# Kernel optimization log

Measured on AMD Instinct MI355X. Metric: run time of the kernel, lower is better.

The kernel has to match this reference:

```python
import jax, jax.numpy as jnp
import numpy as np

N, D = 131072, 512

def setup_inputs() -> dict:
    key = jax.random.key(0)
    kx, = jax.random.split(key, 1)
    X = jax.random.normal(kx, (N, D), dtype=jnp.float32)
    gamma = jnp.ones((D,), dtype=jnp.float32)
    beta = jnp.zeros((D,), dtype=jnp.float32)
    return {"X": X, "gamma": gamma, "beta": beta}

def reference(X, gamma, beta):
    # R = X - mean over rows (samples)
    R = X - jnp.mean(X, axis=0, keepdims=True)            # [N, D]
    # Sigma = diag(R^T @ R) / N  ==  per-feature biased variance
    Sigma = jnp.mean(R * R, axis=0)                       # [D]
    inv_sqrt_Sigma = jax.lax.rsqrt(Sigma)                 # [D] (no epsilon in original)
    Z = R * inv_sqrt_Sigma[None, :]                       # [N, D]
    Y = Z * gamma[None, :] + beta[None, :]                # [N, D]
    return Y
```

## Files before the change

### kernel.cpp

```cpp
#include <hip/hip_runtime.h>
#include <math.h>

#define N_ROWS 131072
#define D_COLS 512
#define TOTAL4 (N_ROWS * D_COLS / 4)

typedef float v4f __attribute__((ext_vector_type(4)));

__global__ __launch_bounds__(512)
void bn_stats_kernel(const v4f* __restrict__ X, float* __restrict__ partial) {
    const int t = threadIdx.x;
    const int g = blockIdx.x * blockDim.x + t;
    const int stride = gridDim.x * blockDim.x;

    v4f s = (v4f)0.0f;
    v4f q = (v4f)0.0f;

    for (int i = g; i < TOTAL4; i += stride) {
        v4f x = X[i];
        s += x;
        q += x * x;
    }

    __shared__ v4f ls[512];
    __shared__ v4f lq[512];
    ls[t] = s;
    lq[t] = q;
    __syncthreads();

    if (t < 256) {
        ls[t] += ls[t + 256];
        lq[t] += lq[t + 256];
    }
    __syncthreads();
    if (t < 128) {
        v4f sv = ls[t] + ls[t + 128];
        v4f qv = lq[t] + lq[t + 128];
        float* dst = partial + (size_t)blockIdx.x * 1024;
        *(v4f*)(dst + 4 * t)       = sv;
        *(v4f*)(dst + 512 + 4 * t) = qv;
    }
}

__global__ __launch_bounds__(256)
void bn_finalize_kernel(const float* __restrict__ partial,
                        const float* __restrict__ gamma,
                        const float* __restrict__ beta,
                        float* __restrict__ scale,
                        float* __restrict__ bias,
                        int B) {
    const int d = blockIdx.x;
    const int t = threadIdx.x;

    float s = 0.f, q = 0.f;
    for (int b = t; b < B; b += blockDim.x) {
        s += partial[(size_t)b * 1024 + d];
        q += partial[(size_t)b * 1024 + 512 + d];
    }

    __shared__ float ls[256];
    __shared__ float lq[256];
    ls[t] = s;
    lq[t] = q;
    __syncthreads();
    for (int off = 128; off > 0; off >>= 1) {
        if (t < off) { ls[t] += ls[t + off]; lq[t] += lq[t + off]; }
        __syncthreads();
    }

    if (t == 0) {
        const float invN = 1.0f / (float)N_ROWS;
        float mean = ls[0] * invN;
        float var  = lq[0] * invN - mean * mean;
        float inv  = rsqrtf(var);
        float sc   = gamma[d] * inv;
        scale[d] = sc;
        bias[d]  = beta[d] - mean * sc;
    }
}

__global__ __launch_bounds__(256)
void bn_norm_kernel(const v4f* __restrict__ X,
                    v4f* __restrict__ Y,
                    const float* __restrict__ scale,
                    const float* __restrict__ bias) {
    const int g = blockIdx.x * blockDim.x + threadIdx.x;
    const int stride = gridDim.x * blockDim.x;
    const int c = (g & 127) * 4;

    const v4f sc = *(const v4f*)(scale + c);
    const v4f bi = *(const v4f*)(bias + c);

    for (int i = g; i < TOTAL4; i += stride) {
        v4f x = X[i];
        v4f y = x * sc + bi;
        __builtin_nontemporal_store(y, &Y[i]);
    }
}

extern "C" void kernel_launch(void* const* d_in, const int* in_sizes, int n_in,
                              void* d_out, int out_size, void* d_ws, size_t ws_size,
                              hipStream_t stream) {
    const float* X     = (const float*)d_in[0];
    const float* gamma = (const float*)d_in[1];
    const float* beta  = (const float*)d_in[2];
    float* Y  = (float*)d_out;
    float* ws = (float*)d_ws;

    int B = 512;
    while (B > 64 && ((size_t)B * 1024 + 1024) * sizeof(float) > ws_size) B >>= 1;

    float* partial = ws;
    float* scale   = ws + (size_t)B * 1024;
    float* bias    = scale + 512;

    bn_stats_kernel<<<B, 512, 0, stream>>>((const v4f*)X, partial);
    bn_finalize_kernel<<<512, 256, 0, stream>>>(partial, gamma, beta, scale, bias, B);
    bn_norm_kernel<<<4096, 256, 0, stream>>>((const v4f*)X, (v4f*)Y, scale, bias);
}
```

Before: 479.0 us.

## Widen stats grid, unroll compile-time loops, vectorize finalize over feature quads

The stats kernel now runs 2048 blocks of 256 threads instead of 512 blocks of 512, with a compile-time trip count and unroll 8 to keep more loads in flight. The finalize kernel handles four features per block using vector loads and writes scale and bias into one packed buffer. The normalize kernel also gets a constant trip count with unroll 4. The wider stats grid means four times as many partial rows for finalize to read, and it needs a larger workspace, falling back to 512 blocks if the workspace is too small.

```diff
diff --git a/kernel.cpp b/kernel.cpp
--- a/kernel.cpp
+++ b/kernel.cpp
@@ -7,32 +7,30 @@
 
 typedef float v4f __attribute__((ext_vector_type(4)));
 
-__global__ __launch_bounds__(512)
+template<int NBLK>
+__global__ __launch_bounds__(256)
 void bn_stats_kernel(const v4f* __restrict__ X, float* __restrict__ partial) {
+    constexpr int STRIDE = NBLK * 256;
+    constexpr int ITERS  = TOTAL4 / STRIDE;
     const int t = threadIdx.x;
-    const int g = blockIdx.x * blockDim.x + t;
-    const int stride = gridDim.x * blockDim.x;
+    const int g = blockIdx.x * 256 + t;
 
     v4f s = (v4f)0.0f;
     v4f q = (v4f)0.0f;
 
-    for (int i = g; i < TOTAL4; i += stride) {
-        v4f x = X[i];
+    #pragma unroll 8
+    for (int k = 0; k < ITERS; ++k) {
+        v4f x = X[g + k * STRIDE];
         s += x;
         q += x * x;
     }
 
-    __shared__ v4f ls[512];
-    __shared__ v4f lq[512];
+    __shared__ v4f ls[256];
+    __shared__ v4f lq[256];
     ls[t] = s;
     lq[t] = q;
     __syncthreads();
 
-    if (t < 256) {
-        ls[t] += ls[t + 256];
-        lq[t] += lq[t + 256];
-    }
-    __syncthreads();
     if (t < 128) {
         v4f sv = ls[t] + ls[t + 128];
         v4f qv = lq[t] + lq[t + 128];
@@ -46,20 +44,20 @@
 void bn_finalize_kernel(const float* __restrict__ partial,
                         const float* __restrict__ gamma,
                         const float* __restrict__ beta,
-                        float* __restrict__ scale,
-                        float* __restrict__ bias,
+                        float* __restrict__ sb,
                         int B) {
-    const int d = blockIdx.x;
-    const int t = threadIdx.x;
+    const int qd = blockIdx.x;
+    const int t  = threadIdx.x;
 
-    float s = 0.f, q = 0.f;
-    for (int b = t; b < B; b += blockDim.x) {
-        s += partial[(size_t)b * 1024 + d];
-        q += partial[(size_t)b * 1024 + 512 + d];
+    v4f s = (v4f)0.0f, q = (v4f)0.0f;
+    for (int b = t; b < B; b += 256) {
+        const float* src = partial + (size_t)b * 1024;
+        s += *(const v4f*)(src + 4 * qd);
+        q += *(const v4f*)(src + 512 + 4 * qd);
     }
 
-    __shared__ float ls[256];
-    __shared__ float lq[256];
+    __shared__ v4f ls[256];
+    __shared__ v4f lq[256];
     ls[t] = s;
     lq[t] = q;
     __syncthreads();
@@ -70,31 +68,41 @@
 
     if (t == 0) {
         const float invN = 1.0f / (float)N_ROWS;
-        float mean = ls[0] * invN;
-        float var  = lq[0] * invN - mean * mean;
-        float inv  = rsqrtf(var);
-        float sc   = gamma[d] * inv;
-        scale[d] = sc;
-        bias[d]  = beta[d] - mean * sc;
+        v4f sv = ls[0], qv = lq[0];
+        v4f mean = sv * invN;
+        v4f var  = qv * invN - mean * mean;
+        v4f inv;
+        inv.x = rsqrtf(var.x);
+        inv.y = rsqrtf(var.y);
+        inv.z = rsqrtf(var.z);
+        inv.w = rsqrtf(var.w);
+        v4f g4 = *(const v4f*)(gamma + 4 * qd);
+        v4f b4 = *(const v4f*)(beta  + 4 * qd);
+        v4f sc = g4 * inv;
+        v4f bi = b4 - mean * sc;
+        *(v4f*)(sb + 4 * qd)       = sc;
+        *(v4f*)(sb + 512 + 4 * qd) = bi;
     }
 }
 
+template<int NBLK>
 __global__ __launch_bounds__(256)
 void bn_norm_kernel(const v4f* __restrict__ X,
                     v4f* __restrict__ Y,
-                    const float* __restrict__ scale,
-                    const float* __restrict__ bias) {
-    const int g = blockIdx.x * blockDim.x + threadIdx.x;
-    const int stride = gridDim.x * blockDim.x;
+                    const float* __restrict__ sb) {
+    constexpr int STRIDE = NBLK * 256;
+    constexpr int ITERS  = TOTAL4 / STRIDE;
+    const int g = blockIdx.x * 256 + threadIdx.x;
     const int c = (g & 127) * 4;
 
-    const v4f sc = *(const v4f*)(scale + c);
-    const v4f bi = *(const v4f*)(bias + c);
+    const v4f sc = *(const v4f*)(sb + c);
+    const v4f bi = *(const v4f*)(sb + 512 + c);
 
-    for (int i = g; i < TOTAL4; i += stride) {
-        v4f x = X[i];
+    #pragma unroll 4
+    for (int k = 0; k < ITERS; ++k) {
+        v4f x = X[g + k * STRIDE];
         v4f y = x * sc + bi;
-        __builtin_nontemporal_store(y, &Y[i]);
+        __builtin_nontemporal_store(y, &Y[g + k * STRIDE]);
     }
 }
 
@@ -107,14 +115,17 @@
     float* Y  = (float*)d_out;
     float* ws = (float*)d_ws;
 
-    int B = 512;
-    while (B > 64 && ((size_t)B * 1024 + 1024) * sizeof(float) > ws_size) B >>= 1;
+    int B = 2048;
+    if (((size_t)B * 1024 + 1024) * sizeof(float) > ws_size) B = 512;
 
     float* partial = ws;
-    float* scale   = ws + (size_t)B * 1024;
-    float* bias    = scale + 512;
+    float* sb      = ws + (size_t)B * 1024;
 
-    bn_stats_kernel<<<B, 512, 0, stream>>>((const v4f*)X, partial);
-    bn_finalize_kernel<<<512, 256, 0, stream>>>(partial, gamma, beta, scale, bias, B);
-    bn_norm_kernel<<<4096, 256, 0, stream>>>((const v4f*)X, (v4f*)Y, scale, bias);
+    if (B == 2048) {
+        bn_stats_kernel<2048><<<2048, 256, 0, stream>>>((const v4f*)X, partial);
+    } else {
+        bn_stats_kernel<512><<<512, 256, 0, stream>>>((const v4f*)X, partial);
+    }
+    bn_finalize_kernel<<<128, 256, 0, stream>>>(partial, gamma, beta, sb, B);
+    bn_norm_kernel<4096><<<4096, 256, 0, stream>>>((const v4f*)X, (v4f*)Y, sb);
 }
```

New measurement: 510.7 us. 1.07x slower.
